# Kernel optimization log

Measured on AMD Instinct MI355X. Metric: run time of the kernel, lower is better.

## Reference

```python
import jax, jax.numpy as jnp
import numpy as np

EPS = 1e-9
# ((top,bottom),(left,right)) zero-pads for the 8 neighbor directions,
# matching torch nn.ZeroPad2d((l,r,t,b)) order gate1..gate8 in the source.
PADS = [((0, 2), (0, 2)), ((0, 2), (1, 1)), ((0, 2), (2, 0)),
        ((1, 1), (0, 2)), ((1, 1), (2, 0)),
        ((2, 0), (0, 2)), ((2, 0), (1, 1)), ((2, 0), (2, 0))]


def _pad8(x):
    # x: (B,H,W) -> (B,8,H+2,W+2): 8 directional zero-padded shifts
    return jnp.stack([jnp.pad(x, ((0, 0), tb, lr)) for tb, lr in PADS], axis=1)


def _affinity_normalization(guidance):
    # guidance: (B,8,H,W) -> gate_wb (B,8,H+2,W+2), gate_sum (B,H,W)
    gate_wb = jnp.stack(
        [jnp.pad(guidance[:, k], ((0, 0), tb, lr)) for k, (tb, lr) in enumerate(PADS)],
        axis=1)
    abs_weight = jnp.sum(jnp.abs(gate_wb), axis=1, keepdims=True)
    gate_wb = gate_wb / (abs_weight + EPS)
    gate_sum = jnp.sum(gate_wb, axis=1)[:, 1:-1, 1:-1]
    return gate_wb, gate_sum


def setup_inputs() -> dict:
    key = jax.random.key(0)
    k1, k2, k3, k4 = jax.random.split(key, 4)
    B, H, W = 2, 384, 1280
    guidance = jax.random.normal(k1, (B, 8, H, W), dtype=jnp.float32)
    blur_depth = jax.random.uniform(k2, (B, 1, H, W), dtype=jnp.float32) * 80.0
    valid = (jax.random.uniform(k3, (B, 1, H, W)) < 0.05).astype(jnp.float32)
    sparse_depth = valid * jax.random.uniform(k4, (B, 1, H, W), dtype=jnp.float32) * 80.0
    return {"guidance": guidance, "blur_depth": blur_depth,
            "sparse_depth": sparse_depth, "prop_time": 24}


def reference(guidance, blur_depth, sparse_depth, prop_time):
    # CSPN affinity-guided iterative propagation (norm_type='8sum')
    gate_wb, gate_sum = _affinity_normalization(guidance)
    raw = blur_depth[:, 0]                       # (B,H,W)
    sparse_mask = jnp.sign(sparse_depth[:, 0])   # (B,H,W), 1 where valid
    d = raw
    for _ in range(prop_time):
        # weighted sum over 8 padded neighbor shifts, then crop halo
        nws = jnp.sum(gate_wb * _pad8(d), axis=1)[:, 1:-1, 1:-1]
        d = (1.0 - gate_sum) * raw + nws
        d = (1.0 - sparse_mask) * d + sparse_mask * raw
    return d  # (B,H,W), matches result_depth.squeeze(1)
```

## Files before the change

kernel.cpp:

```cpp
#include <hip/hip_runtime.h>

static constexpr int Hh = 384;
static constexpr int Ww = 1280;
static constexpr int HW = Hh * Ww;
static constexpr int NPIX = 2 * HW;
static constexpr int TILE_I = 48;
static constexpr int TILE_J = 40;
static constexpr int S_STEPS = 8;
static constexpr int RI = TILE_I + 2 * S_STEPS;
static constexpr int RJ = TILE_J + 2 * S_STEPS;
static constexpr int RR = RI * RJ;
static constexpr int II = RI - 2;
static constexpr int IJ = RJ - 2;
static constexpr int NPAIR_ROW = IJ / 2;
static constexpr int NPAIR = II * NPAIR_ROW;
static constexpr int BLOCK = 512;
static constexpr int PPQ = RR / BLOCK;
static constexpr int PPR = (NPAIR + BLOCK - 1) / BLOCK;
static constexpr int TI_T = Hh / TILE_I;
static constexpr int TJ_T = Ww / TILE_J;
static constexpr int GRID = 2 * TI_T * TJ_T;
static constexpr int NXCD = 8;
static constexpr int CHUNK = GRID / NXCD;
static constexpr float EPSF = 1e-9f;

static constexpr int DI[8] = { 1, 1, 1, 0, 0, -1, -1, -1 };
static constexpr int DJ[8] = { 1, 0, -1, 1, -1, 1, 0, -1 };

static __device__ __forceinline__ int iclamp(int v, int lo, int hi) {
    return min(max(v, lo), hi);
}

template <bool FIRST>
__global__ __launch_bounds__(BLOCK, 2)
void mega(
    const float* __restrict__ g,
    const float* blur,
    const float* __restrict__ sparse,
    const float* din,
    float* __restrict__ dout)
{
    __shared__ float sd[2][RR];

    const int tid = threadIdx.x;
    int bx = ((int)blockIdx.x % NXCD) * CHUNK + (int)blockIdx.x / NXCD;
    const int tj = bx % TJ_T; bx /= TJ_T;
    const int ti = bx % TI_T;
    const int b  = bx / TI_T;
    const int oi = ti * TILE_I - S_STEPS;
    const int oj = tj * TILE_J - S_STEPS;

    const float* blurb = blur + (size_t)b * HW;
    const float* dinb  = (FIRST ? blur : din) + (size_t)b * HW;
    const float* gb    = g + (size_t)b * 8 * HW;

#pragma unroll
    for (int q = 0; q < PPQ; q++) {
        int p = tid + q * BLOCK;
        int ri = p / RJ, rj = p - ri * RJ;
        int gi = iclamp(oi + ri, 0, Hh - 1);
        int gj = iclamp(oj + rj, 0, Ww - 1);
        sd[0][p] = dinb[gi * Ww + gj];
    }

    float2 wp[PPR][8];
    float2 Cc[PPR];
    int    pr[PPR];
#pragma unroll
    for (int q = 0; q < PPR; q++) {
        int pi = tid + q * BLOCK;
        if (pi < NPAIR) {
            int r0 = pi / NPAIR_ROW;
            int c0 = pi - r0 * NPAIR_ROW;
            int ri = 1 + r0;
            int rj = 1 + 2 * c0;
            int p  = ri * RJ + rj;
            int rngr = min(ri, RI - 1 - ri);
            int rng0 = min(rngr, min(rj,     RJ - 1 - rj));
            int rng1 = min(rngr, min(rj + 1, RJ - 2 - rj));
            pr[q] = p | (max(rng0, rng1) << 16);
            float Cv[2], wv[2][8];
#pragma unroll
            for (int x = 0; x < 2; x++) {
                int gi = iclamp(oi + ri, 0, Hh - 1);
                int gj = iclamp(oj + rj + x, 0, Ww - 1);
                float v[8];
                float a = EPSF;
#pragma unroll
                for (int k = 0; k < 8; k++) {
                    int ii = gi + DI[k], jj = gj + DJ[k];
                    float gv = 0.0f;
                    if (ii >= 0 && ii < Hh && jj >= 0 && jj < Ww)
                        gv = gb[k * HW + ii * Ww + jj];
                    v[k] = gv;
                    a += fabsf(gv);
                }
                float inv = 1.0f / a, gs = 0.0f;
#pragma unroll
                for (int k = 0; k < 8; k++) { v[k] *= inv; gs += v[k]; }
                int idx = gi * Ww + gj;
                float rawv = blurb[idx];
                bool m = sparse[b * HW + idx] > 0.0f;
                Cv[x] = m ? rawv : (1.0f - gs) * rawv;
#pragma unroll
                for (int k = 0; k < 8; k++) wv[x][k] = m ? 0.0f : v[k];
            }
            Cc[q] = make_float2(Cv[0], Cv[1]);
#pragma unroll
            for (int k = 0; k < 8; k++)
                wp[q][k] = make_float2(wv[0][k], wv[1][k]);
        } else {
            pr[q] = 0;
            Cc[q] = make_float2(0.0f, 0.0f);
#pragma unroll
            for (int k = 0; k < 8; k++) wp[q][k] = make_float2(0.0f, 0.0f);
        }
    }
    __syncthreads();

    int cur = 0;
#pragma unroll 1
    for (int s = 1; s < S_STEPS; ++s) {
        const float* s0 = sd[cur];
        float* s1 = sd[cur ^ 1];
#pragma unroll
        for (int q = 0; q < PPR; q++) {
            if ((pr[q] >> 16) >= s) {
                int p = pr[q] & 0xffff;
                float2 uA = *(const float2*)(s0 + p - RJ - 1);
                float2 uB = *(const float2*)(s0 + p - RJ + 1);
                float2 mA = *(const float2*)(s0 + p - 1);
                float2 mB = *(const float2*)(s0 + p + 1);
                float2 dA = *(const float2*)(s0 + p + RJ - 1);
                float2 dB = *(const float2*)(s0 + p + RJ + 1);
                float ax = Cc[q].x, ay = Cc[q].y;
                ax = fmaf(wp[q][0].x, dB.x, ax);  ay = fmaf(wp[q][0].y, dB.y, ay);
                ax = fmaf(wp[q][1].x, dA.y, ax);  ay = fmaf(wp[q][1].y, dB.x, ay);
                ax = fmaf(wp[q][2].x, dA.x, ax);  ay = fmaf(wp[q][2].y, dA.y, ay);
                ax = fmaf(wp[q][3].x, mB.x, ax);  ay = fmaf(wp[q][3].y, mB.y, ay);
                ax = fmaf(wp[q][4].x, mA.x, ax);  ay = fmaf(wp[q][4].y, mA.y, ay);
                ax = fmaf(wp[q][5].x, uB.x, ax);  ay = fmaf(wp[q][5].y, uB.y, ay);
                ax = fmaf(wp[q][6].x, uA.y, ax);  ay = fmaf(wp[q][6].y, uB.x, ay);
                ax = fmaf(wp[q][7].x, uA.x, ax);  ay = fmaf(wp[q][7].y, uA.y, ay);
                s1[p]     = ax;
                s1[p + 1] = ay;
            }
        }
        __syncthreads();
        cur ^= 1;
    }

    const float* s0 = sd[cur];
#pragma unroll
    for (int q = 0; q < PPR; q++) {
        if ((pr[q] >> 16) >= S_STEPS) {
            int p = pr[q] & 0xffff;
            float2 uA = *(const float2*)(s0 + p - RJ - 1);
            float2 uB = *(const float2*)(s0 + p - RJ + 1);
            float2 mA = *(const float2*)(s0 + p - 1);
            float2 mB = *(const float2*)(s0 + p + 1);
            float2 dA = *(const float2*)(s0 + p + RJ - 1);
            float2 dB = *(const float2*)(s0 + p + RJ + 1);
            float ax = Cc[q].x, ay = Cc[q].y;
            ax = fmaf(wp[q][0].x, dB.x, ax);  ay = fmaf(wp[q][0].y, dB.y, ay);
            ax = fmaf(wp[q][1].x, dA.y, ax);  ay = fmaf(wp[q][1].y, dB.x, ay);
            ax = fmaf(wp[q][2].x, dA.x, ax);  ay = fmaf(wp[q][2].y, dA.y, ay);
            ax = fmaf(wp[q][3].x, mB.x, ax);  ay = fmaf(wp[q][3].y, mB.y, ay);
            ax = fmaf(wp[q][4].x, mA.x, ax);  ay = fmaf(wp[q][4].y, mA.y, ay);
            ax = fmaf(wp[q][5].x, uB.x, ax);  ay = fmaf(wp[q][5].y, uB.y, ay);
            ax = fmaf(wp[q][6].x, uA.y, ax);  ay = fmaf(wp[q][6].y, uB.x, ay);
            ax = fmaf(wp[q][7].x, uA.x, ax);  ay = fmaf(wp[q][7].y, uA.y, ay);
            int ri = p / RJ, rj = p - ri * RJ;
            int gbase = b * HW + (oi + ri) * Ww + (oj + rj);
            if (rj >= S_STEPS && rj < RJ - S_STEPS)
                dout[gbase]     = ax;
            if (rj + 1 >= S_STEPS && rj + 1 < RJ - S_STEPS)
                dout[gbase + 1] = ay;
        }
    }
}

extern "C" void kernel_launch(void* const* d_in, const int* in_sizes, int n_in,
                              void* d_out, int out_size, void* d_ws, size_t ws_size,
                              hipStream_t stream) {
    const float* guidance = (const float*)d_in[0];
    const float* blur     = (const float*)d_in[1];
    const float* sparse   = (const float*)d_in[2];
    float* out = (float*)d_out;

    char* ws = (char*)d_ws;
    float* bufA = (float*)ws;
    float* bufB = bufA + NPIX;

    mega<true ><<<GRID, BLOCK, 0, stream>>>(guidance, blur, sparse, nullptr, bufA);
    mega<false><<<GRID, BLOCK, 0, stream>>>(guidance, blur, sparse, bufA, bufB);
    mega<false><<<GRID, BLOCK, 0, stream>>>(guidance, blur, sparse, bufB, out);
}
```

Measured before the change: 140.0 us.

## Precompute normalized affinity weights once in fp16 and reuse across propagation launches

Adds a prepass kernel that computes the normalized 8-neighbour weights (stored as fp16) and the constant term per pixel. The three propagation kernels then load these instead of recomputing the normalization from the raw guidance tensor in each launch. This removes redundant guidance reads and arithmetic, but adds a kernel launch and extra workspace traffic, and fp16 weights reduce accuracy.

```diff
diff --git a/kernel.cpp b/kernel.cpp
--- a/kernel.cpp
+++ b/kernel.cpp
@@ -1,4 +1,5 @@
 #include <hip/hip_runtime.h>
+#include <hip/hip_fp16.h>
 
 static constexpr int Hh = 384;
 static constexpr int Ww = 1280;
@@ -24,19 +25,57 @@
 static constexpr int CHUNK = GRID / NXCD;
 static constexpr float EPSF = 1e-9f;
 
-static constexpr int DI[8] = { 1, 1, 1, 0, 0, -1, -1, -1 };
-static constexpr int DJ[8] = { 1, 0, -1, 1, -1, 1, 0, -1 };
+__device__ __constant__ int DI_c[8] = { 1, 1, 1, 0, 0, -1, -1, -1 };
+__device__ __constant__ int DJ_c[8] = { 1, 0, -1, 1, -1, 1, 0, -1 };
 
 static __device__ __forceinline__ int iclamp(int v, int lo, int hi) {
     return min(max(v, lo), hi);
+}
+
+
+__global__ void affinity_norm(const float* __restrict__ g,
+                              const float* __restrict__ raw,
+                              const float* __restrict__ sparse,
+                              __half* __restrict__ wbuf,
+                              float* __restrict__ cbuf) {
+    int idx = blockIdx.x * blockDim.x + threadIdx.x;
+    if (idx >= NPIX) return;
+    int b = idx / HW;
+    int r = idx - b * HW;
+    int i = r / Ww;
+    int j = r - i * Ww;
+
+    const float* gb = g + (size_t)b * 8 * HW;
+    float v[8];
+    float a = EPSF;
+#pragma unroll
+    for (int k = 0; k < 8; k++) {
+        int ii = i + DI_c[k], jj = j + DJ_c[k];
+        float gv = 0.0f;
+        if (ii >= 0 && ii < Hh && jj >= 0 && jj < Ww)
+            gv = gb[k * HW + ii * Ww + jj];
+        v[k] = gv;
+        a += fabsf(gv);
+    }
+    float inv = 1.0f / a, gs = 0.0f;
+#pragma unroll
+    for (int k = 0; k < 8; k++) { v[k] *= inv; gs += v[k]; }
+
+    float rawv = raw[idx];
+    bool m = sparse[idx] > 0.0f;
+    cbuf[idx] = m ? rawv : (1.0f - gs) * rawv;
+    __half wv[8];
+#pragma unroll
+    for (int k = 0; k < 8; k++) wv[k] = __float2half(m ? 0.0f : v[k]);
+    *(float4*)(wbuf + (size_t)idx * 8) = *(const float4*)wv;
 }
 
 template <bool FIRST>
 __global__ __launch_bounds__(BLOCK, 2)
 void mega(
-    const float* __restrict__ g,
+    const __half* __restrict__ wbuf,
+    const float* __restrict__ cbuf,
     const float* blur,
-    const float* __restrict__ sparse,
     const float* din,
     float* __restrict__ dout)
 {
@@ -50,9 +89,7 @@
     const int oi = ti * TILE_I - S_STEPS;
     const int oj = tj * TILE_J - S_STEPS;
 
-    const float* blurb = blur + (size_t)b * HW;
-    const float* dinb  = (FIRST ? blur : din) + (size_t)b * HW;
-    const float* gb    = g + (size_t)b * 8 * HW;
+    const float* dinb = (FIRST ? blur : din) + (size_t)b * HW;
 
 #pragma unroll
     for (int q = 0; q < PPQ; q++) {
@@ -84,26 +121,18 @@
             for (int x = 0; x < 2; x++) {
                 int gi = iclamp(oi + ri, 0, Hh - 1);
                 int gj = iclamp(oj + rj + x, 0, Ww - 1);
-                float v[8];
-                float a = EPSF;
-#pragma unroll
-                for (int k = 0; k < 8; k++) {
-                    int ii = gi + DI[k], jj = gj + DJ[k];
-                    float gv = 0.0f;
-                    if (ii >= 0 && ii < Hh && jj >= 0 && jj < Ww)
-                        gv = gb[k * HW + ii * Ww + jj];
-                    v[k] = gv;
-                    a += fabsf(gv);
-                }
-                float inv = 1.0f / a, gs = 0.0f;
-#pragma unroll
-                for (int k = 0; k < 8; k++) { v[k] *= inv; gs += v[k]; }
-                int idx = gi * Ww + gj;
-                float rawv = blurb[idx];
-                bool m = sparse[b * HW + idx] > 0.0f;
-                Cv[x] = m ? rawv : (1.0f - gs) * rawv;
-#pragma unroll
-                for (int k = 0; k < 8; k++) wv[x][k] = m ? 0.0f : v[k];
+                int idx = b * HW + gi * Ww + gj;
+                float4 w4 = *(const float4*)(wbuf + (size_t)idx * 8);
+                const __half2* wh = (const __half2*)&w4;
+                float2 w01 = __half22float2(wh[0]);
+                float2 w23 = __half22float2(wh[1]);
+                float2 w45 = __half22float2(wh[2]);
+                float2 w67 = __half22float2(wh[3]);
+                wv[x][0] = w01.x; wv[x][1] = w01.y;
+                wv[x][2] = w23.x; wv[x][3] = w23.y;
+                wv[x][4] = w45.x; wv[x][5] = w45.y;
+                wv[x][6] = w67.x; wv[x][7] = w67.y;
+                Cv[x] = cbuf[idx];
             }
             Cc[q] = make_float2(Cv[0], Cv[1]);
 #pragma unroll
@@ -191,8 +220,14 @@
     char* ws = (char*)d_ws;
     float* bufA = (float*)ws;
     float* bufB = bufA + NPIX;
-
-    mega<true ><<<GRID, BLOCK, 0, stream>>>(guidance, blur, sparse, nullptr, bufA);
-    mega<false><<<GRID, BLOCK, 0, stream>>>(guidance, blur, sparse, bufA, bufB);
-    mega<false><<<GRID, BLOCK, 0, stream>>>(guidance, blur, sparse, bufB, out);
-}
+    __half* wbuf = (__half*)(bufB + NPIX);
+    float*  cbuf = (float*)(wbuf + (size_t)NPIX * 8);
+
+    const int threads = 256;
+    const int blocks = (NPIX + threads - 1) / threads;
+    affinity_norm<<<blocks, threads, 0, stream>>>(guidance, blur, sparse, wbuf, cbuf);
+
+    mega<true ><<<GRID, BLOCK, 0, stream>>>(wbuf, cbuf, blur, nullptr, bufA);
+    mega<false><<<GRID, BLOCK, 0, stream>>>(wbuf, cbuf, nullptr, bufA, bufB);
+    mega<false><<<GRID, BLOCK, 0, stream>>>(wbuf, cbuf, nullptr, bufB, out);
+}
```

Result: faster. 129.0 us (-7.9%).
